# Performance work log

Hardware: AMD Instinct MI355X
Metric: run time of the kernel (lower is better)

Reference implementation:

```python
import jax, jax.numpy as jnp
import numpy as np

N = 100000
E = 1600000
IN_DIM = 128
HID = 128
OUT_DIM = 128


def _glorot(key, shape):
    lim = jnp.sqrt(6.0 / (shape[0] + shape[1]))
    return jax.random.uniform(key, shape, jnp.float32, -lim, lim)


def setup_inputs() -> dict:
    key = jax.random.key(0)
    ks = jax.random.split(key, 8)
    x = jax.random.normal(ks[0], (N, IN_DIM), jnp.float32)
    edge_index = jax.random.randint(ks[1], (2, E), 0, N, jnp.int64)
    # layer 1 (SAGEConv(in_dim, hid)): lin_l applied to mean-aggregated neighbors (with bias),
    # lin_r applied to root features (no bias) -- PyG SAGEConv semantics.
    W1l = _glorot(ks[2], (IN_DIM, HID))
    b1l = jnp.zeros((HID,), jnp.float32)
    W1r = _glorot(ks[3], (IN_DIM, HID))
    # layer 2 (SAGEConv(hid, out_dim))
    W2l = _glorot(ks[4], (HID, OUT_DIM))
    b2l = jnp.zeros((OUT_DIM,), jnp.float32)
    W2r = _glorot(ks[5], (HID, OUT_DIM))
    return {"x": x, "edge_index": edge_index,
            "W1l": W1l, "b1l": b1l, "W1r": W1r,
            "W2l": W2l, "b2l": b2l, "W2r": W2r}


def _sage_conv(h, src, dst, Wl, bl, Wr):
    # mean aggregation of source features onto target nodes
    msg_sum = jax.ops.segment_sum(h[src], dst, num_segments=N)  # [N, d]
    deg = jax.ops.segment_sum(jnp.ones((src.shape[0],), h.dtype), dst, num_segments=N)
    agg = msg_sum / jnp.maximum(deg, 1.0)[:, None]
    return agg @ Wl + bl + h @ Wr


def reference(x, edge_index, W1l, b1l, W1r, W2l, b2l, W2r):
    src = edge_index[0]
    dst = edge_index[1]
    h = jax.nn.relu(_sage_conv(x, src, dst, W1l, b1l, W1r))
    h = _sage_conv(h, src, dst, W2l, b2l, W2r)
    return h
```

## Files before the change

kernel.cpp:

```cpp
#include <hip/hip_runtime.h>
#include <cstdint>
#include <cstddef>

#define NN 100000
#define EE 1600000
#define DIM 128
#define CAP 48
#define OVF_CAP 512

#define NB 391
#define BCAP 4608
#define SLOTS 32
#define FLUSH_AT 16
#define ACHUNK 4096

typedef __attribute__((ext_vector_type(8))) short bf16x8;
typedef __attribute__((ext_vector_type(8))) unsigned short u16x8;
typedef __attribute__((ext_vector_type(4))) float f32x4;

__device__ __forceinline__ unsigned short f2bf(float f) {
  union { float f; uint32_t u; } v; v.f = f;
  uint32_t r = v.u + 0x7FFF + ((v.u >> 16) & 1);
  return (unsigned short)(r >> 16);
}
__device__ __forceinline__ float bf2f(unsigned short s) {
  union { uint32_t u; float f; } v; v.u = (uint32_t)s << 16;
  return v.f;
}

__global__ __launch_bounds__(256) void partA_kernel(
    const void* __restrict__ edges, int* __restrict__ bcnt,
    unsigned* __restrict__ part, int* __restrict__ novf, int* __restrict__ ovf) {
  __shared__ unsigned stage[NB][SLOTS + 1];
  __shared__ int scnt[NB];
  __shared__ int sh_i64;
  const int t = threadIdx.x;
  for (int b = t; b < NB; b += 256) scnt[b] = 0;
  if (t < 64) {
    int v = ((const int*)edges)[2 * t + 1];
    unsigned long long m = __ballot(v != 0);
    if (t == 0) sh_i64 = (m == 0ull) ? 1 : 0;
  }
  __syncthreads();
  const int i64 = sh_i64;
  const long long ebase = (long long)blockIdx.x * ACHUNK;
  const int nrounds = ACHUNK / 256;
  for (int r = 0; r < nrounds; ++r) {
    long long e = ebase + (long long)r * 256 + t;
    if (e < EE) {
      int s, d;
      if (i64) {
        s = (int)((const long long*)edges)[e];
        d = (int)((const long long*)edges)[(long long)EE + e];
      } else {
        s = ((const int*)edges)[e];
        d = ((const int*)edges)[(long long)EE + e];
      }
      if ((unsigned)s < NN && (unsigned)d < NN) {
        int b = d >> 8;
        unsigned pk = (unsigned)s | ((unsigned)(d & 255) << 17);
        int pos = atomicAdd(&scnt[b], 1);
        if (pos < SLOTS) {
          stage[b][pos] = pk;
        } else {
          int g = atomicAdd(&bcnt[b], 1);
          if (g < BCAP) part[(size_t)b * BCAP + g] = pk;
          else { int oi = atomicAdd(novf, 1); if (oi < OVF_CAP) { ovf[oi*2] = s; ovf[oi*2+1] = d; } }
        }
      }
    }
    __syncthreads();
    const bool last = (r == nrounds - 1);
    for (int b = t; b < NB; b += 256) {
      int c = scnt[b];
      if (c > SLOTS) c = SLOTS;
      if (c > 0 && (last || c >= FLUSH_AT)) {
        int g = atomicAdd(&bcnt[b], c);
        for (int i = 0; i < c; ++i) {
          int gp = g + i;
          unsigned pk = stage[b][i];
          if (gp < BCAP) {
            part[(size_t)b * BCAP + gp] = pk;
          } else {
            int oi = atomicAdd(novf, 1);
            if (oi < OVF_CAP) { ovf[oi*2] = (int)(pk & 0x1FFFF); ovf[oi*2+1] = (b << 8) | (int)(pk >> 17); }
          }
        }
        scnt[b] = 0;
      }
    }
    __syncthreads();
  }
}

__global__ __launch_bounds__(256) void partB_kernel(
    const int* __restrict__ bcnt, const unsigned* __restrict__ part,
    int* __restrict__ cnt, int* __restrict__ ell,
    int* __restrict__ novf, int* __restrict__ ovf) {
  __shared__ int lcnt[256];
  __shared__ int lell[256 * CAP];
  const int t = threadIdx.x;
  const int b = blockIdx.x;
  lcnt[t] = 0;
  __syncthreads();
  int n = bcnt[b];
  if (n > BCAP) n = BCAP;
  for (int i = t; i < n; i += 256) {
    unsigned pk = part[(size_t)b * BCAP + i];
    int s = (int)(pk & 0x1FFFF);
    int dl = (int)(pk >> 17);
    int pos = atomicAdd(&lcnt[dl], 1);
    if (pos < CAP) lell[dl * CAP + pos] = s;
    else { int oi = atomicAdd(novf, 1); if (oi < OVF_CAP) { ovf[oi*2] = s; ovf[oi*2+1] = (b << 8) | dl; } }
  }
  __syncthreads();
  int4* dst = (int4*)(ell + (size_t)b * 256 * CAP);
  const int4* src = (const int4*)lell;
#pragma unroll
  for (int i = 0; i < 256 * CAP / 4 / 256; ++i) dst[t + i * 256] = src[t + i * 256];
  int node = b * 256 + t;
  if (node < NN) cnt[node] = lcnt[t];
}

__global__ void cast_kernel(const float* __restrict__ x, unsigned short* __restrict__ xhi) {
  int i = blockIdx.x * 256 + threadIdx.x;
  if (i >= NN * DIM / 4) return;
  f32x4 v = ((const f32x4*)x)[i];
  ushort4 hi;
  hi.x = f2bf(v[0]); hi.y = f2bf(v[1]); hi.z = f2bf(v[2]); hi.w = f2bf(v[3]);
  ((ushort4*)xhi)[i] = hi;
}

__global__ __launch_bounds__(256) void gather_ell_kernel(
    const int* __restrict__ cnt, const int* __restrict__ ell,
    const unsigned short* __restrict__ h, unsigned short* __restrict__ ahi,
    const int* __restrict__ novf, const int* __restrict__ ovf) {
  const int node = blockIdx.x * 4 + (threadIdx.x >> 6);
  const int lane = threadIdx.x & 63;
  const int q = lane >> 4;
  const int l = lane & 15;
  if (node >= NN) return;
  const int dcnt = cnt[node];
  const int n = dcnt < CAP ? dcnt : CAP;
  const int* row = ell + (size_t)node * CAP;
  float s[8] = {0.f, 0.f, 0.f, 0.f, 0.f, 0.f, 0.f, 0.f};
  int p = q;
  for (; p + 4 < n; p += 8) {
    u16x8 v0 = *(const u16x8*)(h + (size_t)row[p] * DIM + l * 8);
    u16x8 v1 = *(const u16x8*)(h + (size_t)row[p + 4] * DIM + l * 8);
#pragma unroll
    for (int i = 0; i < 8; ++i) s[i] += bf2f(v0[i]) + bf2f(v1[i]);
  }
  if (p < n) {
    u16x8 v0 = *(const u16x8*)(h + (size_t)row[p] * DIM + l * 8);
#pragma unroll
    for (int i = 0; i < 8; ++i) s[i] += bf2f(v0[i]);
  }
#pragma unroll
  for (int i = 0; i < 8; ++i) {
    s[i] += __shfl_xor(s[i], 16, 64);
    s[i] += __shfl_xor(s[i], 32, 64);
  }
  if (q == 0) {
    if (dcnt > CAP) {
      int no = *novf;
      if (no > OVF_CAP) no = OVF_CAP;
      for (int i = 0; i < no; ++i) {
        if (ovf[i * 2 + 1] == node) {
          u16x8 v0 = *(const u16x8*)(h + (size_t)ovf[i * 2] * DIM + l * 8);
#pragma unroll
          for (int j = 0; j < 8; ++j) s[j] += bf2f(v0[j]);
        }
      }
    }
    const float rd = 1.0f / fmaxf((float)dcnt, 1.0f);
    u16x8 o;
#pragma unroll
    for (int i = 0; i < 8; ++i) o[i] = f2bf(s[i] * rd);
    *(u16x8*)(ahi + (size_t)node * DIM + l * 8) = o;
  }
}

__global__ void wprep_kernel(const float* __restrict__ W1l, const float* __restrict__ W1r,
                             const float* __restrict__ W2l, const float* __restrict__ W2r,
                             unsigned short* __restrict__ Wt1, unsigned short* __restrict__ Wt2) {
  int idx = blockIdx.x * 256 + threadIdx.x;
  int layer = idx >> 15;
  int rest = idx & 32767;
  int mat = rest >> 14;
  int r = rest & 16383;
  int k = r >> 7, n = r & 127;
  const float* W = layer ? (mat ? W2r : W2l) : (mat ? W1r : W1l);
  unsigned short* Wt = layer ? Wt2 : Wt1;
  Wt[((size_t)(mat * 128 + n)) * 128 + k] = f2bf(W[k * 128 + n]);
}

template <bool RELU, bool WPLANES, bool WOUT>
__global__ __launch_bounds__(256, 2) void dense_mfma_kernel(
    const unsigned short* __restrict__ ahi, const unsigned short* __restrict__ hhi,
    const unsigned short* __restrict__ Wt, const float* __restrict__ bl,
    float* __restrict__ out, unsigned short* __restrict__ phi, int n) {
  const int t = threadIdx.x;
  const int wave = t >> 6, lane = t & 63;
  const int l15 = lane & 15, l4 = lane >> 4;
  const int base = blockIdx.x * 64;

  bf16x8 bfr[2][4][2];
#pragma unroll
  for (int mat = 0; mat < 2; ++mat)
#pragma unroll
    for (int kt = 0; kt < 4; ++kt)
#pragma unroll
      for (int ntl = 0; ntl < 2; ++ntl) {
        int ncol = (wave * 2 + ntl) * 16 + l15;
        int k0 = kt * 32 + l4 * 8;
        bfr[mat][kt][ntl] = *(const bf16x8*)(Wt + ((size_t)(mat * 128 + ncol)) * 128 + k0);
      }

  f32x4 acc[4][2];
#pragma unroll
  for (int ntl = 0; ntl < 2; ++ntl) {
    float b = bl[(wave * 2 + ntl) * 16 + l15];
#pragma unroll
    for (int rt = 0; rt < 4; ++rt) {
      f32x4 ib = {b, b, b, b};
      acc[rt][ntl] = ib;
    }
  }

#pragma unroll
  for (int kt = 0; kt < 4; ++kt) {
    const int k0 = kt * 32 + l4 * 8;
#pragma unroll
    for (int rt = 0; rt < 4; ++rt) {
      int row = base + rt * 16 + l15;
      if (row >= n) row = n - 1;
      const size_t off = (size_t)row * DIM + k0;
      bf16x8 a8 = *(const bf16x8*)(ahi + off);
      bf16x8 hh8 = *(const bf16x8*)(hhi + off);
#pragma unroll
      for (int ntl = 0; ntl < 2; ++ntl) {
        acc[rt][ntl] = __builtin_amdgcn_mfma_f32_16x16x32_bf16(a8, bfr[0][kt][ntl], acc[rt][ntl], 0, 0, 0);
        acc[rt][ntl] = __builtin_amdgcn_mfma_f32_16x16x32_bf16(hh8, bfr[1][kt][ntl], acc[rt][ntl], 0, 0, 0);
      }
    }
  }

  __syncthreads();

#pragma unroll
  for (int rt = 0; rt < 4; ++rt)
#pragma unroll
    for (int ntl = 0; ntl < 2; ++ntl) {
      const int col = (wave * 2 + ntl) * 16 + l15;
#pragma unroll
      for (int r = 0; r < 4; ++r) {
        int row = base + rt * 16 + l4 * 4 + r;
        if (row < n) {
          float v = acc[rt][ntl][r];
          if (RELU) v = fmaxf(v, 0.f);
          const size_t off = (size_t)row * DIM + col;
          if (WOUT) out[off] = v;
          if (WPLANES) phi[off] = f2bf(v);
        }
      }
    }
}

extern "C" void kernel_launch(void* const* d_in, const int* in_sizes, int n_in,
                              void* d_out, int out_size, void* d_ws, size_t ws_size,
                              hipStream_t stream) {
  const float* x   = (const float*)d_in[0];
  const void* edges = d_in[1];
  const float* W1l = (const float*)d_in[2];
  const float* b1l = (const float*)d_in[3];
  const float* W1r = (const float*)d_in[4];
  const float* W2l = (const float*)d_in[5];
  const float* b2l = (const float*)d_in[6];
  const float* W2r = (const float*)d_in[7];
  float* out = (float*)d_out;

  char* p = (char*)d_ws;
  unsigned short* Wt1 = (unsigned short*)p;               p += 2 * 128 * 128 * 2;
  unsigned short* Wt2 = (unsigned short*)p;               p += 2 * 128 * 128 * 2;
  int* cnt  = (int*)p;                                    p += (size_t)NN * 4;
  int* bcnt = (int*)p;                                    p += (size_t)NB * 4;
  int* novf = (int*)p;                                    p += 4;
  p = (char*)(((uintptr_t)p + 15) & ~(uintptr_t)15);
  int* ovf = (int*)p;                                     p += (size_t)OVF_CAP * 2 * 4;
  p = (char*)(((uintptr_t)p + 255) & ~(uintptr_t)255);
  int* ell = (int*)p;                                     p += (size_t)NB * 256 * CAP * 4;
  p = (char*)(((uintptr_t)p + 255) & ~(uintptr_t)255);
  unsigned short* hhi = (unsigned short*)p;               p += (size_t)NN * DIM * 2;
  unsigned short* ahi = (unsigned short*)p;               p += (size_t)NN * DIM * 2;
  unsigned* part = (unsigned*)ahi;

  hipMemsetAsync(bcnt, 0, ((size_t)NB + 1) * 4, stream);

  partA_kernel<<<(EE + ACHUNK - 1) / ACHUNK, 256, 0, stream>>>(edges, bcnt, part, novf, ovf);
  partB_kernel<<<NB, 256, 0, stream>>>(bcnt, part, cnt, ell, novf, ovf);

  wprep_kernel<<<256, 256, 0, stream>>>(W1l, W1r, W2l, W2r, Wt1, Wt2);
  cast_kernel<<<(NN * DIM / 4 + 255) / 256, 256, 0, stream>>>(x, hhi);

  const int gather_blocks = (NN + 3) / 4;
  const int dense_blocks = (NN + 63) / 64;

  gather_ell_kernel<<<gather_blocks, 256, 0, stream>>>(cnt, ell, hhi, ahi, novf, ovf);
  dense_mfma_kernel<true, true, false><<<dense_blocks, 256, 0, stream>>>(
      ahi, hhi, Wt1, b1l, out, hhi, NN);

  gather_ell_kernel<<<gather_blocks, 256, 0, stream>>>(cnt, ell, hhi, ahi, novf, ovf);
  dense_mfma_kernel<false, false, true><<<dense_blocks, 256, 0, stream>>>(
      ahi, hhi, Wt2, b2l, out, nullptr, NN);
}
```

Measured before the change: 270.7 us.

## Gather neighbor features in fp8, fuse prep kernels into partition kernel

```diff
diff --git a/kernel.cpp b/kernel.cpp
--- a/kernel.cpp
+++ b/kernel.cpp
@@ -13,29 +13,124 @@
 #define SLOTS 32
 #define FLUSH_AT 16
 #define ACHUNK 4096
+#define ATHREADS 512
+
+#define NPREP_W 128
+#define NPREP_X ((NN * DIM / 4) / ATHREADS)
+
+#if __has_builtin(__builtin_amdgcn_cvt_pk_f32_fp8) && __has_builtin(__builtin_amdgcn_cvt_pk_fp8_f32)
+#define HAVE_FP8 1
+#else
+#define HAVE_FP8 0
+#endif
 
 typedef __attribute__((ext_vector_type(8))) short bf16x8;
-typedef __attribute__((ext_vector_type(8))) unsigned short u16x8;
 typedef __attribute__((ext_vector_type(4))) float f32x4;
+typedef __attribute__((ext_vector_type(2))) float f32x2;
 
 __device__ __forceinline__ unsigned short f2bf(float f) {
   union { float f; uint32_t u; } v; v.f = f;
   uint32_t r = v.u + 0x7FFF + ((v.u >> 16) & 1);
   return (unsigned short)(r >> 16);
 }
-__device__ __forceinline__ float bf2f(unsigned short s) {
-  union { uint32_t u; float f; } v; v.u = (uint32_t)s << 16;
-  return v.f;
-}
-
-__global__ __launch_bounds__(256) void partA_kernel(
+__device__ __forceinline__ uint32_t pk2(float a, float b) {
+  return (uint32_t)f2bf(a) | ((uint32_t)f2bf(b) << 16);
+}
+
+template <bool HI>
+__device__ __forceinline__ uint32_t f2fp8_pair(float a, float b, uint32_t old) {
+#if HAVE_FP8
+  return (uint32_t)__builtin_amdgcn_cvt_pk_fp8_f32(a, b, (int)old, HI);
+#else
+  auto enc = [](float f) -> uint32_t {
+    union { float f; uint32_t u; } v; v.f = f;
+    uint32_t s = (v.u >> 31) << 7;
+    uint32_t m = v.u & 0x7FFFFFFF;
+    if (m < 0x3C000000u) {
+      union { uint32_t u; float f; } w; w.u = m;
+      int q = (int)(w.f * 512.0f + 0.5f);
+      if (q > 7) return s | (1u << 3);
+      return s | (uint32_t)q;
+    }
+    uint32_t u2 = m + 0x00080000u;
+    int e = (int)(u2 >> 23) - 127;
+    if (e > 8) return s | 0x7E;
+    return s | ((uint32_t)(e + 7) << 3) | ((u2 >> 20) & 7);
+  };
+  uint32_t pr = enc(a) | (enc(b) << 8);
+  return HI ? ((old & 0x0000FFFFu) | (pr << 16)) : ((old & 0xFFFF0000u) | pr);
+#endif
+}
+
+__device__ __forceinline__ void acc_fp8x8(float* s, uint2 w) {
+#if HAVE_FP8
+  f32x2 f;
+  f = __builtin_amdgcn_cvt_pk_f32_fp8((int)w.x, false); s[0] += f.x; s[1] += f.y;
+  f = __builtin_amdgcn_cvt_pk_f32_fp8((int)w.x, true);  s[2] += f.x; s[3] += f.y;
+  f = __builtin_amdgcn_cvt_pk_f32_fp8((int)w.y, false); s[4] += f.x; s[5] += f.y;
+  f = __builtin_amdgcn_cvt_pk_f32_fp8((int)w.y, true);  s[6] += f.x; s[7] += f.y;
+#else
+  auto dec = [](uint32_t b) -> float {
+    uint32_t sg = (b >> 7) & 1, e = (b >> 3) & 15, m = b & 7;
+    if (e == 0) return (sg ? -1.f : 1.f) * (float)m * 0.001953125f;
+    union { uint32_t u; float f; } w;
+    w.u = (sg << 31) | ((e + 120) << 23) | (m << 20);
+    return w.f;
+  };
+#pragma unroll
+  for (int i = 0; i < 4; ++i) s[i] += dec((w.x >> (i * 8)) & 0xFF);
+#pragma unroll
+  for (int i = 0; i < 4; ++i) s[4 + i] += dec((w.y >> (i * 8)) & 0xFF);
+#endif
+}
+
+__device__ __forceinline__ bf16x8 cvt8(f32x4 a, f32x4 b) {
+  union { uint32_t u[4]; bf16x8 v; } r;
+  asm("v_cvt_pk_bf16_f32 %0, %1, %2" : "=v"(r.u[0]) : "v"(a[0]), "v"(a[1]));
+  asm("v_cvt_pk_bf16_f32 %0, %1, %2" : "=v"(r.u[1]) : "v"(a[2]), "v"(a[3]));
+  asm("v_cvt_pk_bf16_f32 %0, %1, %2" : "=v"(r.u[2]) : "v"(b[0]), "v"(b[1]));
+  asm("v_cvt_pk_bf16_f32 %0, %1, %2" : "=v"(r.u[3]) : "v"(b[2]), "v"(b[3]));
+  return r.v;
+}
+
+__global__ __launch_bounds__(ATHREADS) void partA_prep_kernel(
     const void* __restrict__ edges, int* __restrict__ bcnt,
-    unsigned* __restrict__ part, int* __restrict__ novf, int* __restrict__ ovf) {
+    unsigned* __restrict__ part, int* __restrict__ novf, int* __restrict__ ovf,
+    const float* __restrict__ x,
+    const float* __restrict__ W1l, const float* __restrict__ W1r,
+    const float* __restrict__ W2l, const float* __restrict__ W2r,
+    unsigned short* __restrict__ Wt1, unsigned short* __restrict__ Wt2,
+    unsigned char* __restrict__ x8) {
   __shared__ unsigned stage[NB][SLOTS + 1];
   __shared__ int scnt[NB];
   __shared__ int sh_i64;
   const int t = threadIdx.x;
-  for (int b = t; b < NB; b += 256) scnt[b] = 0;
+
+  if (blockIdx.x >= NB) {
+    int bid = blockIdx.x - NB;
+    if (bid < NPREP_W) {
+      int idx = bid * ATHREADS + t;
+      int layer = idx >> 15;
+      int rest = idx & 32767;
+      int mat = rest >> 14;
+      int r = rest & 16383;
+      int k = r >> 7, n = r & 127;
+      const float* W = layer ? (mat ? W2r : W2l) : (mat ? W1r : W1l);
+      unsigned short* Wt = layer ? Wt2 : Wt1;
+      Wt[((size_t)(mat * 128 + n)) * 128 + k] = f2bf(W[k * 128 + n]);
+    } else {
+      int i = (bid - NPREP_W) * ATHREADS + t;
+      if (i < NN * DIM / 4) {
+        f32x4 v = ((const f32x4*)x)[i];
+        uint32_t pk = f2fp8_pair<false>(v[0], v[1], 0);
+        pk = f2fp8_pair<true>(v[2], v[3], pk);
+        ((uint32_t*)x8)[i] = pk;
+      }
+    }
+    return;
+  }
+
+  for (int b = t; b < NB; b += ATHREADS) scnt[b] = 0;
   if (t < 64) {
     int v = ((const int*)edges)[2 * t + 1];
     unsigned long long m = __ballot(v != 0);
@@ -44,9 +139,9 @@
   __syncthreads();
   const int i64 = sh_i64;
   const long long ebase = (long long)blockIdx.x * ACHUNK;
-  const int nrounds = ACHUNK / 256;
+  const int nrounds = ACHUNK / ATHREADS;
   for (int r = 0; r < nrounds; ++r) {
-    long long e = ebase + (long long)r * 256 + t;
+    long long e = ebase + (long long)r * ATHREADS + t;
     if (e < EE) {
       int s, d;
       if (i64) {
@@ -71,7 +166,7 @@
     }
     __syncthreads();
     const bool last = (r == nrounds - 1);
-    for (int b = t; b < NB; b += 256) {
+    for (int b = t; b < NB; b += ATHREADS) {
       int c = scnt[b];
       if (c > SLOTS) c = SLOTS;
       if (c > 0 && (last || c >= FLUSH_AT)) {
@@ -122,18 +217,9 @@
   if (node < NN) cnt[node] = lcnt[t];
 }
 
-__global__ void cast_kernel(const float* __restrict__ x, unsigned short* __restrict__ xhi) {
-  int i = blockIdx.x * 256 + threadIdx.x;
-  if (i >= NN * DIM / 4) return;
-  f32x4 v = ((const f32x4*)x)[i];
-  ushort4 hi;
-  hi.x = f2bf(v[0]); hi.y = f2bf(v[1]); hi.z = f2bf(v[2]); hi.w = f2bf(v[3]);
-  ((ushort4*)xhi)[i] = hi;
-}
-
 __global__ __launch_bounds__(256) void gather_ell_kernel(
     const int* __restrict__ cnt, const int* __restrict__ ell,
-    const unsigned short* __restrict__ h, unsigned short* __restrict__ ahi,
+    const unsigned char* __restrict__ h8, unsigned short* __restrict__ ahi,
     const int* __restrict__ novf, const int* __restrict__ ovf) {
   const int node = blockIdx.x * 4 + (threadIdx.x >> 6);
   const int lane = threadIdx.x & 63;
@@ -145,16 +231,19 @@
   const int* row = ell + (size_t)node * CAP;
   float s[8] = {0.f, 0.f, 0.f, 0.f, 0.f, 0.f, 0.f, 0.f};
   int p = q;
-  for (; p + 4 < n; p += 8) {
-    u16x8 v0 = *(const u16x8*)(h + (size_t)row[p] * DIM + l * 8);
-    u16x8 v1 = *(const u16x8*)(h + (size_t)row[p + 4] * DIM + l * 8);
-#pragma unroll
-    for (int i = 0; i < 8; ++i) s[i] += bf2f(v0[i]) + bf2f(v1[i]);
-  }
-  if (p < n) {
-    u16x8 v0 = *(const u16x8*)(h + (size_t)row[p] * DIM + l * 8);
-#pragma unroll
-    for (int i = 0; i < 8; ++i) s[i] += bf2f(v0[i]);
+  for (; p + 12 < n; p += 16) {
+    uint2 w0 = *(const uint2*)(h8 + (size_t)row[p] * DIM + l * 8);
+    uint2 w1 = *(const uint2*)(h8 + (size_t)row[p + 4] * DIM + l * 8);
+    uint2 w2 = *(const uint2*)(h8 + (size_t)row[p + 8] * DIM + l * 8);
+    uint2 w3 = *(const uint2*)(h8 + (size_t)row[p + 12] * DIM + l * 8);
+    acc_fp8x8(s, w0);
+    acc_fp8x8(s, w1);
+    acc_fp8x8(s, w2);
+    acc_fp8x8(s, w3);
+  }
+  for (; p < n; p += 4) {
+    uint2 w0 = *(const uint2*)(h8 + (size_t)row[p] * DIM + l * 8);
+    acc_fp8x8(s, w0);
   }
 #pragma unroll
   for (int i = 0; i < 8; ++i) {
@@ -167,39 +256,26 @@
       if (no > OVF_CAP) no = OVF_CAP;
       for (int i = 0; i < no; ++i) {
         if (ovf[i * 2 + 1] == node) {
-          u16x8 v0 = *(const u16x8*)(h + (size_t)ovf[i * 2] * DIM + l * 8);
-#pragma unroll
-          for (int j = 0; j < 8; ++j) s[j] += bf2f(v0[j]);
+          uint2 w0 = *(const uint2*)(h8 + (size_t)ovf[i * 2] * DIM + l * 8);
+          acc_fp8x8(s, w0);
         }
       }
     }
     const float rd = 1.0f / fmaxf((float)dcnt, 1.0f);
-    u16x8 o;
-#pragma unroll
-    for (int i = 0; i < 8; ++i) o[i] = f2bf(s[i] * rd);
-    *(u16x8*)(ahi + (size_t)node * DIM + l * 8) = o;
-  }
-}
-
-__global__ void wprep_kernel(const float* __restrict__ W1l, const float* __restrict__ W1r,
-                             const float* __restrict__ W2l, const float* __restrict__ W2r,
-                             unsigned short* __restrict__ Wt1, unsigned short* __restrict__ Wt2) {
-  int idx = blockIdx.x * 256 + threadIdx.x;
-  int layer = idx >> 15;
-  int rest = idx & 32767;
-  int mat = rest >> 14;
-  int r = rest & 16383;
-  int k = r >> 7, n = r & 127;
-  const float* W = layer ? (mat ? W2r : W2l) : (mat ? W1r : W1l);
-  unsigned short* Wt = layer ? Wt2 : Wt1;
-  Wt[((size_t)(mat * 128 + n)) * 128 + k] = f2bf(W[k * 128 + n]);
-}
-
-template <bool RELU, bool WPLANES, bool WOUT>
+    uint4 o;
+    o.x = pk2(s[0] * rd, s[1] * rd);
+    o.y = pk2(s[2] * rd, s[3] * rd);
+    o.z = pk2(s[4] * rd, s[5] * rd);
+    o.w = pk2(s[6] * rd, s[7] * rd);
+    *(uint4*)(ahi + (size_t)node * DIM + l * 8) = o;
+  }
+}
+
+template <bool RELU, bool WFP8>
 __global__ __launch_bounds__(256, 2) void dense_mfma_kernel(
-    const unsigned short* __restrict__ ahi, const unsigned short* __restrict__ hhi,
+    const unsigned short* __restrict__ ahi, const float* h,
     const unsigned short* __restrict__ Wt, const float* __restrict__ bl,
-    float* __restrict__ out, unsigned short* __restrict__ phi, int n) {
+    float* out, unsigned char* __restrict__ ph8, int n) {
   const int t = threadIdx.x;
   const int wave = t >> 6, lane = t & 63;
   const int l15 = lane & 15, l4 = lane >> 4;
@@ -237,7 +313,9 @@
       if (row >= n) row = n - 1;
       const size_t off = (size_t)row * DIM + k0;
       bf16x8 a8 = *(const bf16x8*)(ahi + off);
-      bf16x8 hh8 = *(const bf16x8*)(hhi + off);
+      f32x4 h0 = *(const f32x4*)(h + off);
+      f32x4 h1 = *(const f32x4*)(h + off + 4);
+      bf16x8 hh8 = cvt8(h0, h1);
 #pragma unroll
       for (int ntl = 0; ntl < 2; ++ntl) {
         acc[rt][ntl] = __builtin_amdgcn_mfma_f32_16x16x32_bf16(a8, bfr[0][kt][ntl], acc[rt][ntl], 0, 0, 0);
@@ -260,8 +338,8 @@
           float v = acc[rt][ntl][r];
           if (RELU) v = fmaxf(v, 0.f);
           const size_t off = (size_t)row * DIM + col;
-          if (WOUT) out[off] = v;
-          if (WPLANES) phi[off] = f2bf(v);
+          out[off] = v;
+          if (WFP8) ph8[off] = (unsigned char)(f2fp8_pair<false>(v, v, 0) & 0xFF);
         }
       }
     }
@@ -291,26 +369,25 @@
   p = (char*)(((uintptr_t)p + 255) & ~(uintptr_t)255);
   int* ell = (int*)p;                                     p += (size_t)NB * 256 * CAP * 4;
   p = (char*)(((uintptr_t)p + 255) & ~(uintptr_t)255);
-  unsigned short* hhi = (unsigned short*)p;               p += (size_t)NN * DIM * 2;
   unsigned short* ahi = (unsigned short*)p;               p += (size_t)NN * DIM * 2;
-  unsigned* part = (unsigned*)ahi;
-
-  hipMemsetAsync(bcnt, 0, ((size_t)NB + 1) * 4, stream);
-
-  partA_kernel<<<(EE + ACHUNK - 1) / ACHUNK, 256, 0, stream>>>(edges, bcnt, part, novf, ovf);
+  unsigned char* x8 = (unsigned char*)p;                  p += (size_t)NN * DIM;
+  unsigned char* h8 = (unsigned char*)p;                  p += (size_t)NN * DIM;
+  unsigned* part = (unsigned*)h8;
+
+  (void)hipMemsetAsync(bcnt, 0, ((size_t)NB + 1) * 4, stream);
+
+  partA_prep_kernel<<<NB + NPREP_W + NPREP_X, ATHREADS, 0, stream>>>(
+      edges, bcnt, part, novf, ovf, x, W1l, W1r, W2l, W2r, Wt1, Wt2, x8);
   partB_kernel<<<NB, 256, 0, stream>>>(bcnt, part, cnt, ell, novf, ovf);
-
-  wprep_kernel<<<256, 256, 0, stream>>>(W1l, W1r, W2l, W2r, Wt1, Wt2);
-  cast_kernel<<<(NN * DIM / 4 + 255) / 256, 256, 0, stream>>>(x, hhi);
 
   const int gather_blocks = (NN + 3) / 4;
   const int dense_blocks = (NN + 63) / 64;
 
-  gather_ell_kernel<<<gather_blocks, 256, 0, stream>>>(cnt, ell, hhi, ahi, novf, ovf);
-  dense_mfma_kernel<true, true, false><<<dense_blocks, 256, 0, stream>>>(
-      ahi, hhi, Wt1, b1l, out, hhi, NN);
-
-  gather_ell_kernel<<<gather_blocks, 256, 0, stream>>>(cnt, ell, hhi, ahi, novf, ovf);
-  dense_mfma_kernel<false, false, true><<<dense_blocks, 256, 0, stream>>>(
-      ahi, hhi, Wt2, b2l, out, nullptr, NN);
-}
+  gather_ell_kernel<<<gather_blocks, 256, 0, stream>>>(cnt, ell, x8, ahi, novf, ovf);
+  dense_mfma_kernel<true, true><<<dense_blocks, 256, 0, stream>>>(
+      ahi, x, Wt1, b1l, out, h8, NN);
+
+  gather_ell_kernel<<<gather_blocks, 256, 0, stream>>>(cnt, ell, h8, ahi, novf, ovf);
+  dense_mfma_kernel<false, false><<<dense_blocks, 256, 0, stream>>>(
+      ahi, out, Wt2, b2l, out, nullptr, NN);
+}
```

Measured after the change: 252.7 us. 1.07x faster.
